# Kernel optimization log

Hardware: AMD Instinct MI355X
Metric: run time of the kernel (lower is better)

The kernel has to match this reference:

```python
import jax, jax.numpy as jnp
import numpy as np

D = 256      # d_model
H = 2 * D    # hidden_size = 512
L = 3        # num_layers
VS = 32000   # src vocab
VT = 32000   # tgt vocab
B, S, T = 32, 128, 64


def setup_inputs() -> dict:
    key = jax.random.key(0)
    ks = jax.random.split(key, 24)
    sc = 0.05
    n = lambda k, shp: sc * jax.random.normal(k, shp, dtype=jnp.float32)
    inp = {
        'x': jax.random.randint(ks[0], (B, S), 0, VS, dtype=jnp.int32),
        'y': jax.random.randint(ks[1], (B, T), 0, VT, dtype=jnp.int32),
        'src_emb': n(ks[2], (VS, D)),
        'tgt_emb': n(ks[3], (VT, H)),
        # encoder bi-LSTM: layer 0 (input D), layers 1-2 (input 2D); dim0=dir for e0, (layer,dir) for e12
        'W_ih_e0': n(ks[4], (2, 4 * D, D)),
        'W_hh_e0': n(ks[5], (2, 4 * D, D)),
        'b_e0': n(ks[6], (2, 4 * D)),
        'W_ih_e12': n(ks[7], (2, 2, 4 * D, 2 * D)),
        'W_hh_e12': n(ks[8], (2, 2, 4 * D, D)),
        'b_e12': n(ks[9], (2, 2, 4 * D)),
        # decoder LSTM: layer 0 input = 2*H (embed + attention context), layers 1-2 input H
        'W_ih_d0': n(ks[10], (4 * H, 2 * H)),
        'W_hh_d0': n(ks[11], (4 * H, H)),
        'b_d0': n(ks[12], (4 * H)),
        'W_ih_d12': n(ks[13], (2, 4 * H, H)),
        'W_hh_d12': n(ks[14], (2, 4 * H, H)),
        'b_d12': n(ks[15], (2, 4 * H)),
        # Luong 'general' attention and output head
        'W_a': n(ks[16], (H, H)),
        'W_out': n(ks[17], (VT, H)),
        'b_out': n(ks[18], (VT,)),
    }
    return inp


def lstm_cell(x, h, c, Wih, Whh, b):
    g = x @ Wih.T + h @ Whh.T + b          # [B, 4H'] gates in torch order i,f,g,o
    i, f, gg, o = jnp.split(g, 4, axis=-1)
    c2 = jax.nn.sigmoid(f) * c + jax.nn.sigmoid(i) * jnp.tanh(gg)
    h2 = jax.nn.sigmoid(o) * jnp.tanh(c2)
    return h2, c2


def run_dir(seq, Wih, Whh, b, reverse):
    # seq: [S, B, in]; returns outputs [S, B, Hdir], final (h, c)
    bsz = seq.shape[1]
    hdir = Whh.shape[1]
    h0 = jnp.zeros((bsz, hdir), seq.dtype)
    def step(carry, xt):
        h, c = carry
        h2, c2 = lstm_cell(xt, h, c, Wih, Whh, b)
        return (h2, c2), h2
    (hF, cF), outs = jax.lax.scan(step, (h0, h0), seq, reverse=reverse)
    return outs, hF, cF


def _forward(x, y, src_emb, tgt_emb, W_ih_e0, W_hh_e0, b_e0, W_ih_e12, W_hh_e12, b_e12,
             W_ih_d0, W_hh_d0, b_d0, W_ih_d12, W_hh_d12, b_d12, W_a, W_out, b_out):
    # ---- encoder: 3-layer bidirectional LSTM (dropout=0 at inference) ----
    seq = src_emb[x].transpose(1, 0, 2)  # [S, B, D] time-major
    hs_f, hs_b, cs_f, cs_b = [], [], [], []
    of, hf, cf = run_dir(seq, W_ih_e0[0], W_hh_e0[0], b_e0[0], False)
    ob, hb, cb = run_dir(seq, W_ih_e0[1], W_hh_e0[1], b_e0[1], True)
    hs_f.append(hf); hs_b.append(hb); cs_f.append(cf); cs_b.append(cb)
    seq = jnp.concatenate([of, ob], axis=-1)  # [S, B, 2D]
    for l in range(2):
        of, hf, cf = run_dir(seq, W_ih_e12[l, 0], W_hh_e12[l, 0], b_e12[l, 0], False)
        ob, hb, cb = run_dir(seq, W_ih_e12[l, 1], W_hh_e12[l, 1], b_e12[l, 1], True)
        hs_f.append(hf); hs_b.append(hb); cs_f.append(cf); cs_b.append(cb)
        seq = jnp.concatenate([of, ob], axis=-1)
    enc_seq = seq  # [S, B, H]
    # combine_bidirectional: concat fwd/bwd final states per layer -> [L, B, H]
    h_dec = jnp.stack([jnp.concatenate([hs_f[l], hs_b[l]], -1) for l in range(L)])
    c_dec = jnp.stack([jnp.concatenate([cs_f[l], cs_b[l]], -1) for l in range(L)])

    # ---- decoder: per-timestep attention + 3 stacked LSTM cells + output head ----
    toks = y[:, :-1].T  # [T-1, B] teacher-forced inputs (y[:,0] .. y[:,T-2])
    def dec_step(carry, tok):
        h, c = carry  # [L, B, H]
        emb = tgt_emb[tok]  # [B, H]
        # Luong 'general' attention on previous top-layer hidden
        scores = jnp.einsum('bd,de,sbe->bs', h[-1], W_a, enc_seq)
        attn = jax.nn.softmax(scores, axis=-1)
        ctx = jnp.einsum('bs,sbe->be', attn, enc_seq)  # [B, H]
        inp = jnp.concatenate([emb, ctx], axis=-1)     # [B, 2H]
        h0n, c0n = lstm_cell(inp, h[0], c[0], W_ih_d0, W_hh_d0, b_d0)
        hs, cs, cur = [h0n], [c0n], h0n
        for l in range(2):
            hn, cn = lstm_cell(cur, h[l + 1], c[l + 1], W_ih_d12[l], W_hh_d12[l], b_d12[l])
            hs.append(hn); cs.append(cn); cur = hn
        logits = cur @ W_out.T + b_out  # [B, VT]
        return (jnp.stack(hs), jnp.stack(cs)), logits
    _, logits = jax.lax.scan(dec_step, (h_dec, c_dec), toks)
    return logits.transpose(1, 0, 2)  # [B, T-1, VT]


def reference(x, y, src_emb, tgt_emb, W_ih_e0, W_hh_e0, b_e0, W_ih_e12, W_hh_e12, b_e12,
              W_ih_d0, W_hh_d0, b_d0, W_ih_d12, W_hh_d12, b_d12, W_a, W_out, b_out):
    return _forward(x, y, src_emb, tgt_emb, W_ih_e0, W_hh_e0, b_e0, W_ih_e12, W_hh_e12, b_e12,
                    W_ih_d0, W_hh_d0, b_d0, W_ih_d12, W_hh_d12, b_d12, W_a, W_out, b_out)
```

## Files before the change

### kernel.cpp

```cpp
#include <hip/hip_runtime.h>
#include <hip/hip_bf16.h>

#define B_ 32
#define S_ 128
#define VT_ 32000

typedef __hip_bfloat16 bf16;
typedef short bf16x8 __attribute__((ext_vector_type(8)));
typedef float f32x4 __attribute__((ext_vector_type(4)));

__device__ __forceinline__ float b2f(bf16 v){ return __bfloat162float(v); }
__device__ __forceinline__ float sigf(float x){ return 1.f/(1.f + expf(-x)); }

__global__ __launch_bounds__(256) void k_cvt(const float* __restrict__ src,
                                             bf16* __restrict__ dst, int n)
{
    int i = (blockIdx.x*256 + threadIdx.x)*4;
    if (i >= n) return;
    float4 v = *(const float4*)(src + i);
    dst[i+0] = __float2bfloat16(v.x);
    dst[i+1] = __float2bfloat16(v.y);
    dst[i+2] = __float2bfloat16(v.z);
    dst[i+3] = __float2bfloat16(v.w);
}

__global__ __launch_bounds__(256) void k_embed(const int* __restrict__ x,
                                               const float* __restrict__ emb,
                                               float* __restrict__ outA)
{
    int idx = blockIdx.x*256 + threadIdx.x;
    int row = idx >> 8, d = idx & 255;
    int s = row >> 5, bb = row & 31;
    int tok = x[bb*128 + s];
    outA[(size_t)row*256 + d] = emb[(size_t)tok*256 + d];
}

__global__ __launch_bounds__(256) void k_xgemm(const float* __restrict__ A, int lda, int K,
                                               const float* __restrict__ Wih,
                                               const float* __restrict__ bias,
                                               float* __restrict__ C)
{
    int dir = blockIdx.z;
    const float* W = Wih + (size_t)dir*1024*K;
    const float* bs = bias + dir*1024;
    float* Cd = C + (size_t)dir*4194304;
    __shared__ __align__(16) float As[16][68];
    __shared__ __align__(16) float Ws[16][68];
    int tid = threadIdx.x;
    int m0 = blockIdx.y*64, n0 = blockIdx.x*64;
    int tx = tid & 15, ty = tid >> 4;
    int mr = tid >> 2, kq = tid & 3;
    float acc[4][4];
    #pragma unroll
    for (int i=0;i<4;i++)
        #pragma unroll
        for (int j=0;j<4;j++) acc[i][j] = 0.f;

    for (int k0 = 0; k0 < K; k0 += 16){
        __syncthreads();
        float4 av = *(const float4*)(A + (size_t)(m0+mr)*lda + k0 + kq*4);
        As[kq*4+0][mr] = av.x; As[kq*4+1][mr] = av.y;
        As[kq*4+2][mr] = av.z; As[kq*4+3][mr] = av.w;
        float4 wv = *(const float4*)(W + (size_t)(n0+mr)*K + k0 + kq*4);
        Ws[kq*4+0][mr] = wv.x; Ws[kq*4+1][mr] = wv.y;
        Ws[kq*4+2][mr] = wv.z; Ws[kq*4+3][mr] = wv.w;
        __syncthreads();
        #pragma unroll
        for (int k = 0; k < 16; k++){
            float4 aa = *(const float4*)&As[k][tx*4];
            float4 ww = *(const float4*)&Ws[k][ty*4];
            float a4[4] = {aa.x, aa.y, aa.z, aa.w};
            float w4[4] = {ww.x, ww.y, ww.z, ww.w};
            #pragma unroll
            for (int i=0;i<4;i++)
                #pragma unroll
                for (int j=0;j<4;j++) acc[i][j] += a4[i]*w4[j];
        }
    }
    #pragma unroll
    for (int j=0;j<4;j++){
        float bv = bs[n0 + ty*4 + j];
        #pragma unroll
        for (int i=0;i<4;i++)
            Cd[(size_t)(m0+tx*4+i)*1024 + n0 + ty*4 + j] = acc[i][j] + bv;
    }
}

__global__ __launch_bounds__(256) void k_encscan(const float* __restrict__ xg,
                                                 const bf16* __restrict__ Whh,
                                                 float* __restrict__ outSeq,
                                                 float* __restrict__ hfin,
                                                 float* __restrict__ cfin)
{
    int blk = blockIdx.x;
    int dir = blk >> 5, b = blk & 31;
    int tid = threadIdx.x;
    const bf16* W = Whh + (size_t)dir*262144;
    const float* xgd = xg + (size_t)dir*4194304;
    __shared__ __align__(16) float hs[256];
    hs[tid] = 0.f;
    float c = 0.f, hcur = 0.f;
    __syncthreads();
    const bf16* w0 = W + (size_t)tid*256;
    const bf16* w1 = W + (size_t)(256+tid)*256;
    const bf16* w2 = W + (size_t)(512+tid)*256;
    const bf16* w3 = W + (size_t)(768+tid)*256;
    for (int t = 0; t < 128; t++){
        int td = dir ? (127 - t) : t;
        const float* xr = xgd + (size_t)(td*32 + b)*1024;
        float g0 = xr[tid], g1 = xr[256+tid], g2 = xr[512+tid], g3 = xr[768+tid];
        for (int k = 0; k < 256; k += 8){
            float4 h0 = *(const float4*)&hs[k];
            float4 h1 = *(const float4*)&hs[k+4];
            bf16x8 wa = *(const bf16x8*)(w0 + k);
            bf16x8 wb = *(const bf16x8*)(w1 + k);
            bf16x8 wc = *(const bf16x8*)(w2 + k);
            bf16x8 wd = *(const bf16x8*)(w3 + k);
            float hv[8] = {h0.x, h0.y, h0.z, h0.w, h1.x, h1.y, h1.z, h1.w};
            #pragma unroll
            for (int j=0;j<8;j++){
                float wva, wvb, wvc, wvd;
                {
                    unsigned sa = (unsigned)(unsigned short)wa[j] << 16; wva = __uint_as_float(sa);
                    unsigned sb = (unsigned)(unsigned short)wb[j] << 16; wvb = __uint_as_float(sb);
                    unsigned sc = (unsigned)(unsigned short)wc[j] << 16; wvc = __uint_as_float(sc);
                    unsigned sd = (unsigned)(unsigned short)wd[j] << 16; wvd = __uint_as_float(sd);
                }
                g0 += wva*hv[j]; g1 += wvb*hv[j]; g2 += wvc*hv[j]; g3 += wvd*hv[j];
            }
        }
        float cn = sigf(g1)*c + sigf(g0)*tanhf(g2);
        float hn = sigf(g3)*tanhf(cn);
        c = cn;
        __syncthreads();
        hs[tid] = hn;
        outSeq[(size_t)(td*32 + b)*512 + dir*256 + tid] = hn;
        __syncthreads();
        hcur = hn;
    }
    hfin[(size_t)(dir*32 + b)*256 + tid] = hcur;
    cfin[(size_t)(dir*32 + b)*256 + tid] = c;
}

__global__ __launch_bounds__(256) void k_decinit(const float* __restrict__ hfin,
                                                 const float* __restrict__ cfin,
                                                 bf16* __restrict__ dec_hb,
                                                 float* __restrict__ dec_c)
{
    int idx = blockIdx.x*256 + threadIdx.x;
    int l = idx / 16384;
    int r = idx - l*16384;
    int b = r >> 9, u = r & 511;
    int dir = u >> 8, dd = u & 255;
    size_t src = (size_t)(l*2 + dir)*8192 + b*256 + dd;
    dec_hb[idx] = __float2bfloat16(hfin[src]);
    dec_c[idx] = cfin[src];
}

__global__ __launch_bounds__(256) void k_attn(const bf16* __restrict__ htop,
                                              const float* __restrict__ Wa,
                                              const float* __restrict__ enc,
                                              const int* __restrict__ y,
                                              const float* __restrict__ temb,
                                              bf16* __restrict__ x0, int t)
{
    int b = blockIdx.x, tid = threadIdx.x;
    __shared__ __align__(16) float hsh[512];
    __shared__ float hw[512];
    __shared__ float ps[128];
    __shared__ float red[64];
    hsh[tid]       = b2f(htop[b*512 + tid]);
    hsh[256 + tid] = b2f(htop[b*512 + 256 + tid]);
    __syncthreads();
    float a0 = 0.f, a1 = 0.f;
    for (int d = 0; d < 512; d++){
        float hv = hsh[d];
        a0 += hv * Wa[(size_t)d*512 + tid];
        a1 += hv * Wa[(size_t)d*512 + 256 + tid];
    }
    hw[tid] = a0; hw[256+tid] = a1;
    __syncthreads();
    if (tid < 128){
        const float* er = enc + (size_t)(tid*32 + b)*512;
        float s = 0.f;
        for (int e = 0; e < 512; e++) s += hw[e]*er[e];
        ps[tid] = s;
    }
    __syncthreads();
    if (tid < 64) red[tid] = fmaxf(ps[tid], ps[tid+64]);
    __syncthreads();
    if (tid == 0){ float m = red[0]; for (int i=1;i<64;i++) m = fmaxf(m, red[i]); red[0] = m; }
    __syncthreads();
    float mx = red[0];
    if (tid < 128) ps[tid] = expf(ps[tid] - mx);
    __syncthreads();
    if (tid < 64) red[tid] = ps[tid] + ps[tid+64];
    __syncthreads();
    if (tid == 0){ float ssum = 0.f; for (int i=0;i<64;i++) ssum += red[i]; red[0] = 1.f/ssum; }
    __syncthreads();
    float inv = red[0];
    float c0 = 0.f, c1 = 0.f;
    for (int s2 = 0; s2 < 128; s2++){
        float pv = ps[s2] * inv;
        const float* er = enc + (size_t)(s2*32 + b)*512;
        c0 += pv * er[tid];
        c1 += pv * er[256 + tid];
    }
    int tok = y[b*64 + t];
    x0[b*1024 + tid]       = __float2bfloat16(temb[(size_t)tok*512 + tid]);
    x0[b*1024 + 256 + tid] = __float2bfloat16(temb[(size_t)tok*512 + 256 + tid]);
    x0[b*1024 + 512 + tid] = __float2bfloat16(c0);
    x0[b*1024 + 768 + tid] = __float2bfloat16(c1);
}

__global__ __launch_bounds__(256) void k_decgate(const bf16* __restrict__ X, int Kx,
                                                 const bf16* __restrict__ Hb,
                                                 const bf16* __restrict__ Wih,
                                                 const bf16* __restrict__ Whh,
                                                 const float* __restrict__ bias,
                                                 float* __restrict__ cbuf,
                                                 bf16* __restrict__ hout,
                                                 bf16* __restrict__ hs_out)
{
    int uc = blockIdx.x;
    int tid = threadIdx.x;
    int w = tid >> 6, lane = tid & 63;
    int n = lane & 15, quad = lane >> 4;
    int u0 = uc * 16;
    int KxT = Kx >> 5;
    int KT = KxT + 16;
    int ktpw = KT >> 2;
    const f32x4 fz = {0.f, 0.f, 0.f, 0.f};
    f32x4 acc[2][4];
    #pragma unroll
    for (int mt=0; mt<2; mt++)
        #pragma unroll
        for (int g=0; g<4; g++) acc[mt][g] = fz;
    int koff = quad * 8;
    for (int kt = w*ktpw; kt < (w+1)*ktpw; kt++){
        const bf16* asrc; const bf16* wsrc; int k0, ldk;
        if (kt < KxT){ asrc = X;  wsrc = Wih; k0 = kt << 5;          ldk = Kx;  }
        else         { asrc = Hb; wsrc = Whh; k0 = (kt - KxT) << 5;  ldk = 512; }
        bf16x8 a0 = *(const bf16x8*)(asrc + (size_t)n*ldk + k0 + koff);
        bf16x8 a1 = *(const bf16x8*)(asrc + (size_t)(16+n)*ldk + k0 + koff);
        #pragma unroll
        for (int g = 0; g < 4; g++){
            bf16x8 bv = *(const bf16x8*)(wsrc + (size_t)(g*512 + u0 + n)*ldk + k0 + koff);
            acc[0][g] = __builtin_amdgcn_mfma_f32_16x16x32_bf16(a0, bv, acc[0][g], 0, 0, 0);
            acc[1][g] = __builtin_amdgcn_mfma_f32_16x16x32_bf16(a1, bv, acc[1][g], 0, 0, 0);
        }
    }
    __shared__ float part[4][64][32];
    #pragma unroll
    for (int mt=0; mt<2; mt++)
        #pragma unroll
        for (int g=0; g<4; g++)
            #pragma unroll
            for (int r=0; r<4; r++)
                part[w][lane][(mt*4+g)*4 + r] = acc[mt][g][r];
    __syncthreads();
    for (int pi = tid; pi < 512; pi += 256){
        int b = pi >> 4, ul = pi & 15;
        int mt = b >> 4, reg = b & 3, q = (b >> 2) & 3;
        int ln = q*16 + ul;
        int u = u0 + ul;
        float gv[4];
        #pragma unroll
        for (int g=0; g<4; g++){
            int ix = (mt*4+g)*4 + reg;
            gv[g] = part[0][ln][ix] + part[1][ln][ix] + part[2][ln][ix] + part[3][ln][ix]
                  + bias[g*512 + u];
        }
        float cp = cbuf[b*512 + u];
        float cn = sigf(gv[1])*cp + sigf(gv[0])*tanhf(gv[2]);
        float hn = sigf(gv[3])*tanhf(cn);
        cbuf[b*512 + u] = cn;
        bf16 hb2 = __float2bfloat16(hn);
        hout[b*512 + u] = hb2;
        if (hs_out) hs_out[b*512 + u] = hb2;
    }
}

__global__ __launch_bounds__(256) void k_logits(const bf16* __restrict__ A,
                                                const float* __restrict__ W,
                                                const float* __restrict__ bias,
                                                float* __restrict__ out)
{
    __shared__ __align__(16) bf16 As[64][40];
    __shared__ __align__(16) bf16 Bs[64][40];
    int tid = threadIdx.x;
    int n0 = blockIdx.x * 64;
    int m0 = blockIdx.y * 64;
    int w = tid >> 6, lane = tid & 63;
    int wm = w & 1, wn = w >> 1;
    int q = lane >> 4, nn = lane & 15;
    const f32x4 fz = {0.f, 0.f, 0.f, 0.f};
    f32x4 acc[2][2];
    acc[0][0] = fz; acc[0][1] = fz; acc[1][0] = fz; acc[1][1] = fz;
    int mrow = tid >> 2, kq = tid & 3;
    for (int k0 = 0; k0 < 512; k0 += 32){
        __syncthreads();
        *(uint4*)(&As[mrow][kq*8]) = *(const uint4*)(A + (size_t)(m0+mrow)*512 + k0 + kq*8);
        {
            const float* wp = W + (size_t)(n0+mrow)*512 + k0 + kq*8;
            float4 w0v = *(const float4*)wp;
            float4 w1v = *(const float4*)(wp + 4);
            bf16* bp = &Bs[mrow][kq*8];
            bp[0] = __float2bfloat16(w0v.x); bp[1] = __float2bfloat16(w0v.y);
            bp[2] = __float2bfloat16(w0v.z); bp[3] = __float2bfloat16(w0v.w);
            bp[4] = __float2bfloat16(w1v.x); bp[5] = __float2bfloat16(w1v.y);
            bp[6] = __float2bfloat16(w1v.z); bp[7] = __float2bfloat16(w1v.w);
        }
        __syncthreads();
        #pragma unroll
        for (int mt=0; mt<2; mt++){
            bf16x8 av = *(const bf16x8*)(&As[wm*32 + mt*16 + nn][q*8]);
            #pragma unroll
            for (int nt=0; nt<2; nt++){
                bf16x8 bv = *(const bf16x8*)(&Bs[wn*32 + nt*16 + nn][q*8]);
                acc[mt][nt] = __builtin_amdgcn_mfma_f32_16x16x32_bf16(av, bv, acc[mt][nt], 0, 0, 0);
            }
        }
    }
    #pragma unroll
    for (int mt=0; mt<2; mt++)
        #pragma unroll
        for (int nt=0; nt<2; nt++){
            int ncol = n0 + wn*32 + nt*16 + nn;
            float biasv = bias[ncol];
            #pragma unroll
            for (int r=0; r<4; r++){
                int row = m0 + wm*32 + mt*16 + q*4 + r;
                if (row < 2016){
                    int tt = row >> 5, b = row & 31;
                    out[(size_t)(b*63 + tt)*VT_ + ncol] = acc[mt][nt][r] + biasv;
                }
            }
        }
}

extern "C" void kernel_launch(void* const* d_in, const int* in_sizes, int n_in,
                              void* d_out, int out_size, void* d_ws, size_t ws_size,
                              hipStream_t stream)
{
    (void)in_sizes; (void)n_in; (void)out_size; (void)ws_size;
    const int*   x        = (const int*)d_in[0];
    const int*   y        = (const int*)d_in[1];
    const float* src_emb  = (const float*)d_in[2];
    const float* tgt_emb  = (const float*)d_in[3];
    const float* W_ih_e0  = (const float*)d_in[4];
    const float* W_hh_e0  = (const float*)d_in[5];
    const float* b_e0     = (const float*)d_in[6];
    const float* W_ih_e12 = (const float*)d_in[7];
    const float* W_hh_e12 = (const float*)d_in[8];
    const float* b_e12    = (const float*)d_in[9];
    const float* W_ih_d0  = (const float*)d_in[10];
    const float* W_hh_d0  = (const float*)d_in[11];
    const float* b_d0     = (const float*)d_in[12];
    const float* W_ih_d12 = (const float*)d_in[13];
    const float* W_hh_d12 = (const float*)d_in[14];
    const float* b_d12    = (const float*)d_in[15];
    const float* W_a      = (const float*)d_in[16];
    const float* W_out    = (const float*)d_in[17];
    const float* b_out    = (const float*)d_in[18];

    char* p = (char*)d_ws;
    float* encA   = (float*)p;  p += (size_t)128*32*512*4;
    float* encB   = (float*)p;  p += (size_t)128*32*512*4;
    float* xg     = (float*)p;  p += (size_t)2*128*32*1024*4;
    float* hfin   = (float*)p;  p += (size_t)3*2*32*256*4;
    float* cfin   = (float*)p;  p += (size_t)3*2*32*256*4;
    bf16*  dec_hb = (bf16*)p;   p += (size_t)2*3*32*512*2;
    float* dec_c  = (float*)p;  p += (size_t)3*32*512*4;
    bf16*  x0     = (bf16*)p;   p += (size_t)32*1024*2;
    bf16*  Hs     = (bf16*)p;   p += (size_t)2048*512*2;
    bf16*  wb16   = (bf16*)p;   p += (size_t)8912896*2;

    bf16* whh_e0_b  = wb16;
    bf16* whh_e12_b = wb16 + 524288;
    bf16* wih_d0_b  = wb16 + 1572864;
    bf16* whh_d0_b  = wb16 + 3670016;
    bf16* wih_d12_b = wb16 + 4718592;
    bf16* whh_d12_b = wb16 + 6815744;

    k_cvt<<<512,  256, 0, stream>>>(W_hh_e0,  whh_e0_b,  524288);
    k_cvt<<<1024, 256, 0, stream>>>(W_hh_e12, whh_e12_b, 1048576);
    k_cvt<<<2048, 256, 0, stream>>>(W_ih_d0,  wih_d0_b,  2097152);
    k_cvt<<<1024, 256, 0, stream>>>(W_hh_d0,  whh_d0_b,  1048576);
    k_cvt<<<2048, 256, 0, stream>>>(W_ih_d12, wih_d12_b, 2097152);
    k_cvt<<<2048, 256, 0, stream>>>(W_hh_d12, whh_d12_b, 2097152);

    k_embed<<<4096, 256, 0, stream>>>(x, src_emb, encA);

    k_xgemm<<<dim3(16,64,2), 256, 0, stream>>>(encA, 256, 256, W_ih_e0, b_e0, xg);
    k_encscan<<<64, 256, 0, stream>>>(xg, whh_e0_b, encB, hfin, cfin);
    k_xgemm<<<dim3(16,64,2), 256, 0, stream>>>(encB, 512, 512, W_ih_e12, b_e12, xg);
    k_encscan<<<64, 256, 0, stream>>>(xg, whh_e12_b, encA, hfin + 16384, cfin + 16384);
    k_xgemm<<<dim3(16,64,2), 256, 0, stream>>>(encA, 512, 512, W_ih_e12 + 2*1024*512,
                                               b_e12 + 2048, xg);
    k_encscan<<<64, 256, 0, stream>>>(xg, whh_e12_b + 524288, encB,
                                      hfin + 32768, cfin + 32768);

    k_decinit<<<192, 256, 0, stream>>>(hfin, cfin, dec_hb, dec_c);

    for (int t = 0; t < 63; t++){
        int pp = t & 1, pn = 1 - pp;
        bf16* hbp = dec_hb + (size_t)pp*49152;
        bf16* hbn = dec_hb + (size_t)pn*49152;
        k_attn<<<32, 256, 0, stream>>>(hbp + 32768, W_a, encB, y, tgt_emb, x0, t);
        k_decgate<<<32, 256, 0, stream>>>(x0, 1024, hbp, wih_d0_b, whh_d0_b, b_d0,
                                          dec_c, hbn, (bf16*)nullptr);
        k_decgate<<<32, 256, 0, stream>>>(hbn, 512, hbp + 16384,
                                          wih_d12_b, whh_d12_b, b_d12,
                                          dec_c + 16384, hbn + 16384, (bf16*)nullptr);
        k_decgate<<<32, 256, 0, stream>>>(hbn + 16384, 512, hbp + 32768,
                                          wih_d12_b + 1048576, whh_d12_b + 1048576,
                                          b_d12 + 2048,
                                          dec_c + 32768, hbn + 32768, Hs + (size_t)t*16384);
    }

    k_logits<<<dim3(500,32), 256, 0, stream>>>(Hs, W_out, b_out, (float*)d_out);
}
```

Before: 12.60 ms.

## Fuse decoder time loop into persistent kernel and precompute enc·W_a

The 63-step decoder loop, four launches per step, becomes a single persistent kernel of 32 blocks. The steps are kept in order by a software grid barrier built on an atomic counter that k_decinit resets. The Luong attention is reassociated: enc_seq is multiplied by W_a once with a generalized k_xgemm, so each step only needs dot products with the precomputed encW instead of a 512x512 matvec per batch row. This removes about 250 kernel launches and the repeated W_a reads. In exchange it adds spin-wait barriers, relies on all 32 blocks being resident at once, and costs an extra 8MB workspace buffer.

```diff
diff --git a/kernel.cpp b/kernel.cpp
--- a/kernel.cpp
+++ b/kernel.cpp
@@ -36,14 +36,13 @@
 }
 
 __global__ __launch_bounds__(256) void k_xgemm(const float* __restrict__ A, int lda, int K,
-                                               const float* __restrict__ Wih,
+                                               const float* __restrict__ W,
                                                const float* __restrict__ bias,
-                                               float* __restrict__ C)
+                                               float* __restrict__ C, int N)
 {
     int dir = blockIdx.z;
-    const float* W = Wih + (size_t)dir*1024*K;
-    const float* bs = bias + dir*1024;
-    float* Cd = C + (size_t)dir*4194304;
+    const float* Wd = W + (size_t)dir*N*K;
+    float* Cd = C + (size_t)dir*4096*N;
     __shared__ __align__(16) float As[16][68];
     __shared__ __align__(16) float Ws[16][68];
     int tid = threadIdx.x;
@@ -61,7 +60,7 @@
         float4 av = *(const float4*)(A + (size_t)(m0+mr)*lda + k0 + kq*4);
         As[kq*4+0][mr] = av.x; As[kq*4+1][mr] = av.y;
         As[kq*4+2][mr] = av.z; As[kq*4+3][mr] = av.w;
-        float4 wv = *(const float4*)(W + (size_t)(n0+mr)*K + k0 + kq*4);
+        float4 wv = *(const float4*)(Wd + (size_t)(n0+mr)*K + k0 + kq*4);
         Ws[kq*4+0][mr] = wv.x; Ws[kq*4+1][mr] = wv.y;
         Ws[kq*4+2][mr] = wv.z; Ws[kq*4+3][mr] = wv.w;
         __syncthreads();
@@ -79,10 +78,10 @@
     }
     #pragma unroll
     for (int j=0;j<4;j++){
-        float bv = bs[n0 + ty*4 + j];
+        float bv = bias ? bias[dir*N + n0 + ty*4 + j] : 0.f;
         #pragma unroll
         for (int i=0;i<4;i++)
-            Cd[(size_t)(m0+tx*4+i)*1024 + n0 + ty*4 + j] = acc[i][j] + bv;
+            Cd[(size_t)(m0+tx*4+i)*N + n0 + ty*4 + j] = acc[i][j] + bv;
     }
 }
 
@@ -145,9 +144,11 @@
 __global__ __launch_bounds__(256) void k_decinit(const float* __restrict__ hfin,
                                                  const float* __restrict__ cfin,
                                                  bf16* __restrict__ dec_hb,
-                                                 float* __restrict__ dec_c)
+                                                 float* __restrict__ dec_c,
+                                                 unsigned* __restrict__ bar)
 {
     int idx = blockIdx.x*256 + threadIdx.x;
+    if (idx == 0) *bar = 0;
     int l = idx / 16384;
     int r = idx - l*16384;
     int b = r >> 9, u = r & 511;
@@ -157,73 +158,26 @@
     dec_c[idx] = cfin[src];
 }
 
-__global__ __launch_bounds__(256) void k_attn(const bf16* __restrict__ htop,
-                                              const float* __restrict__ Wa,
-                                              const float* __restrict__ enc,
-                                              const int* __restrict__ y,
-                                              const float* __restrict__ temb,
-                                              bf16* __restrict__ x0, int t)
-{
-    int b = blockIdx.x, tid = threadIdx.x;
-    __shared__ __align__(16) float hsh[512];
-    __shared__ float hw[512];
-    __shared__ float ps[128];
-    __shared__ float red[64];
-    hsh[tid]       = b2f(htop[b*512 + tid]);
-    hsh[256 + tid] = b2f(htop[b*512 + 256 + tid]);
+__device__ __forceinline__ void gbar(unsigned* bar, unsigned target)
+{
     __syncthreads();
-    float a0 = 0.f, a1 = 0.f;
-    for (int d = 0; d < 512; d++){
-        float hv = hsh[d];
-        a0 += hv * Wa[(size_t)d*512 + tid];
-        a1 += hv * Wa[(size_t)d*512 + 256 + tid];
-    }
-    hw[tid] = a0; hw[256+tid] = a1;
+    if (threadIdx.x == 0){
+        __threadfence();
+        __hip_atomic_fetch_add(bar, 1u, __ATOMIC_RELAXED, __HIP_MEMORY_SCOPE_AGENT);
+        while (__hip_atomic_load(bar, __ATOMIC_RELAXED, __HIP_MEMORY_SCOPE_AGENT) < target)
+            __builtin_amdgcn_s_sleep(2);
+        __threadfence();
+    }
     __syncthreads();
-    if (tid < 128){
-        const float* er = enc + (size_t)(tid*32 + b)*512;
-        float s = 0.f;
-        for (int e = 0; e < 512; e++) s += hw[e]*er[e];
-        ps[tid] = s;
-    }
-    __syncthreads();
-    if (tid < 64) red[tid] = fmaxf(ps[tid], ps[tid+64]);
-    __syncthreads();
-    if (tid == 0){ float m = red[0]; for (int i=1;i<64;i++) m = fmaxf(m, red[i]); red[0] = m; }
-    __syncthreads();
-    float mx = red[0];
-    if (tid < 128) ps[tid] = expf(ps[tid] - mx);
-    __syncthreads();
-    if (tid < 64) red[tid] = ps[tid] + ps[tid+64];
-    __syncthreads();
-    if (tid == 0){ float ssum = 0.f; for (int i=0;i<64;i++) ssum += red[i]; red[0] = 1.f/ssum; }
-    __syncthreads();
-    float inv = red[0];
-    float c0 = 0.f, c1 = 0.f;
-    for (int s2 = 0; s2 < 128; s2++){
-        float pv = ps[s2] * inv;
-        const float* er = enc + (size_t)(s2*32 + b)*512;
-        c0 += pv * er[tid];
-        c1 += pv * er[256 + tid];
-    }
-    int tok = y[b*64 + t];
-    x0[b*1024 + tid]       = __float2bfloat16(temb[(size_t)tok*512 + tid]);
-    x0[b*1024 + 256 + tid] = __float2bfloat16(temb[(size_t)tok*512 + 256 + tid]);
-    x0[b*1024 + 512 + tid] = __float2bfloat16(c0);
-    x0[b*1024 + 768 + tid] = __float2bfloat16(c1);
-}
-
-__global__ __launch_bounds__(256) void k_decgate(const bf16* __restrict__ X, int Kx,
-                                                 const bf16* __restrict__ Hb,
-                                                 const bf16* __restrict__ Wih,
-                                                 const bf16* __restrict__ Whh,
-                                                 const float* __restrict__ bias,
-                                                 float* __restrict__ cbuf,
-                                                 bf16* __restrict__ hout,
-                                                 bf16* __restrict__ hs_out)
-{
-    int uc = blockIdx.x;
-    int tid = threadIdx.x;
+}
+
+__device__ __forceinline__ void dec_gate(int uc, int tid,
+    const bf16* __restrict__ X, int Kx, const bf16* __restrict__ Hb,
+    const bf16* __restrict__ Wih, const bf16* __restrict__ Whh,
+    const float* __restrict__ bias,
+    float* __restrict__ cbuf, bf16* __restrict__ hout, bf16* __restrict__ hs_out,
+    float (*part)[64][32])
+{
     int w = tid >> 6, lane = tid & 63;
     int n = lane & 15, quad = lane >> 4;
     int u0 = uc * 16;
@@ -250,7 +204,7 @@
             acc[1][g] = __builtin_amdgcn_mfma_f32_16x16x32_bf16(a1, bv, acc[1][g], 0, 0, 0);
         }
     }
-    __shared__ float part[4][64][32];
+    __syncthreads();
     #pragma unroll
     for (int mt=0; mt<2; mt++)
         #pragma unroll
@@ -278,6 +232,95 @@
         bf16 hb2 = __float2bfloat16(hn);
         hout[b*512 + u] = hb2;
         if (hs_out) hs_out[b*512 + u] = hb2;
+    }
+}
+
+__global__ __launch_bounds__(256) void k_decoder(
+    const bf16* __restrict__ wih0,  const bf16* __restrict__ whh0,  const float* __restrict__ bias0,
+    const bf16* __restrict__ wih12, const bf16* __restrict__ whh12, const float* __restrict__ bias12,
+    const float* __restrict__ encW, const float* __restrict__ enc,
+    const int* __restrict__ y, const float* __restrict__ temb,
+    bf16* __restrict__ dec_hb, float* __restrict__ dec_c,
+    bf16* __restrict__ x0, bf16* __restrict__ Hs, unsigned* bar)
+{
+    int blk = blockIdx.x;
+    int tid = threadIdx.x;
+
+    __shared__ __align__(16) float partA[4][64][32];
+    __shared__ __align__(16) float hsA[512];
+    __shared__ float ps2[256];
+    __shared__ float psA[128];
+    __shared__ float redA[1];
+
+    for (int t = 0; t < 63; t++){
+        int pp = t & 1, pn = 1 - pp;
+        bf16* hbp = dec_hb + (size_t)pp*49152;
+        bf16* hbn = dec_hb + (size_t)pn*49152;
+
+        {
+            const bf16* htp = hbp + 32768 + blk*512;
+            hsA[tid]     = b2f(htp[tid]);
+            hsA[256+tid] = b2f(htp[256+tid]);
+            __syncthreads();
+            {
+                int s = tid & 127, hf = tid >> 7;
+                const float* ew = encW + (size_t)(s*32 + blk)*512 + hf*256;
+                const float* hv = hsA + hf*256;
+                float a0 = 0.f, a1 = 0.f, a2 = 0.f, a3 = 0.f;
+                for (int d = 0; d < 256; d += 4){
+                    a0 += hv[d]*ew[d];     a1 += hv[d+1]*ew[d+1];
+                    a2 += hv[d+2]*ew[d+2]; a3 += hv[d+3]*ew[d+3];
+                }
+                ps2[hf*128 + s] = (a0+a1) + (a2+a3);
+            }
+            __syncthreads();
+            if (tid < 128) psA[tid] = ps2[tid] + ps2[128+tid];
+            __syncthreads();
+            if (tid < 64){
+                float v = fmaxf(psA[tid], psA[tid+64]);
+                #pragma unroll
+                for (int o=32;o>0;o>>=1) v = fmaxf(v, __shfl_xor(v, o));
+                if (tid == 0) redA[0] = v;
+            }
+            __syncthreads();
+            float mx = redA[0];
+            if (tid < 128) psA[tid] = expf(psA[tid] - mx);
+            __syncthreads();
+            if (tid < 64){
+                float v = psA[tid] + psA[tid+64];
+                #pragma unroll
+                for (int o=32;o>0;o>>=1) v += __shfl_xor(v, o);
+                if (tid == 0) redA[0] = 1.f/v;
+            }
+            __syncthreads();
+            float inv = redA[0];
+            float c0 = 0.f, c1 = 0.f;
+            for (int s2 = 0; s2 < 128; s2++){
+                float pv = psA[s2] * inv;
+                const float* er = enc + (size_t)(s2*32 + blk)*512;
+                c0 += pv * er[tid];
+                c1 += pv * er[256 + tid];
+            }
+            int tok = y[blk*64 + t];
+            x0[blk*1024 + tid]       = __float2bfloat16(temb[(size_t)tok*512 + tid]);
+            x0[blk*1024 + 256 + tid] = __float2bfloat16(temb[(size_t)tok*512 + 256 + tid]);
+            x0[blk*1024 + 512 + tid] = __float2bfloat16(c0);
+            x0[blk*1024 + 768 + tid] = __float2bfloat16(c1);
+        }
+        gbar(bar, (unsigned)(t*4 + 1)*32);
+
+        dec_gate(blk, tid, x0, 1024, hbp, wih0, whh0, bias0,
+                 dec_c, hbn, (bf16*)nullptr, partA);
+        gbar(bar, (unsigned)(t*4 + 2)*32);
+
+        dec_gate(blk, tid, hbn, 512, hbp + 16384, wih12, whh12, bias12,
+                 dec_c + 16384, hbn + 16384, (bf16*)nullptr, partA);
+        gbar(bar, (unsigned)(t*4 + 3)*32);
+
+        dec_gate(blk, tid, hbn + 16384, 512, hbp + 32768,
+                 wih12 + 1048576, whh12 + 1048576, bias12 + 2048,
+                 dec_c + 32768, hbn + 32768, Hs + (size_t)t*16384, partA);
+        gbar(bar, (unsigned)(t*4 + 4)*32);
     }
 }
 
@@ -374,6 +417,8 @@
     float* dec_c  = (float*)p;  p += (size_t)3*32*512*4;
     bf16*  x0     = (bf16*)p;   p += (size_t)32*1024*2;
     bf16*  Hs     = (bf16*)p;   p += (size_t)2048*512*2;
+    float* encW   = (float*)p;  p += (size_t)128*32*512*4;
+    unsigned* bar = (unsigned*)p; p += 256;
     bf16*  wb16   = (bf16*)p;   p += (size_t)8912896*2;
 
     bf16* whh_e0_b  = wb16;
@@ -392,32 +437,24 @@
 
     k_embed<<<4096, 256, 0, stream>>>(x, src_emb, encA);
 
-    k_xgemm<<<dim3(16,64,2), 256, 0, stream>>>(encA, 256, 256, W_ih_e0, b_e0, xg);
+    k_xgemm<<<dim3(16,64,2), 256, 0, stream>>>(encA, 256, 256, W_ih_e0, b_e0, xg, 1024);
     k_encscan<<<64, 256, 0, stream>>>(xg, whh_e0_b, encB, hfin, cfin);
-    k_xgemm<<<dim3(16,64,2), 256, 0, stream>>>(encB, 512, 512, W_ih_e12, b_e12, xg);
+    k_xgemm<<<dim3(16,64,2), 256, 0, stream>>>(encB, 512, 512, W_ih_e12, b_e12, xg, 1024);
     k_encscan<<<64, 256, 0, stream>>>(xg, whh_e12_b, encA, hfin + 16384, cfin + 16384);
     k_xgemm<<<dim3(16,64,2), 256, 0, stream>>>(encA, 512, 512, W_ih_e12 + 2*1024*512,
-                                               b_e12 + 2048, xg);
+                                               b_e12 + 2048, xg, 1024);
     k_encscan<<<64, 256, 0, stream>>>(xg, whh_e12_b + 524288, encB,
                                       hfin + 32768, cfin + 32768);
 
-    k_decinit<<<192, 256, 0, stream>>>(hfin, cfin, dec_hb, dec_c);
-
-    for (int t = 0; t < 63; t++){
-        int pp = t & 1, pn = 1 - pp;
-        bf16* hbp = dec_hb + (size_t)pp*49152;
-        bf16* hbn = dec_hb + (size_t)pn*49152;
-        k_attn<<<32, 256, 0, stream>>>(hbp + 32768, W_a, encB, y, tgt_emb, x0, t);
-        k_decgate<<<32, 256, 0, stream>>>(x0, 1024, hbp, wih_d0_b, whh_d0_b, b_d0,
-                                          dec_c, hbn, (bf16*)nullptr);
-        k_decgate<<<32, 256, 0, stream>>>(hbn, 512, hbp + 16384,
-                                          wih_d12_b, whh_d12_b, b_d12,
-                                          dec_c + 16384, hbn + 16384, (bf16*)nullptr);
-        k_decgate<<<32, 256, 0, stream>>>(hbn + 16384, 512, hbp + 32768,
-                                          wih_d12_b + 1048576, whh_d12_b + 1048576,
-                                          b_d12 + 2048,
-                                          dec_c + 32768, hbn + 32768, Hs + (size_t)t*16384);
-    }
+    k_xgemm<<<dim3(8,64,1), 256, 0, stream>>>(encB, 512, 512, W_a,
+                                              (const float*)nullptr, encW, 512);
+
+    k_decinit<<<192, 256, 0, stream>>>(hfin, cfin, dec_hb, dec_c, bar);
+
+    k_decoder<<<32, 256, 0, stream>>>(wih_d0_b, whh_d0_b, b_d0,
+                                      wih_d12_b, whh_d12_b, b_d12,
+                                      encW, encB, y, tgt_emb,
+                                      dec_hb, dec_c, x0, Hs, bar);
 
     k_logits<<<dim3(500,32), 256, 0, stream>>>(Hs, W_out, b_out, (float*)d_out);
 }
```

Result: faster. 11.28 ms (-10.4%).
